# Kernel tuning notes

Hardware: AMD Instinct MI355X
Metric: run time of the kernel (lower is better)

Reference implementation:

```python
import jax, jax.numpy as jnp
import numpy as np
from jax import lax

K = 8          # num_classes
C_IN = 256     # in_channels
EPS = 1e-5


def resize_bilinear_ac(x, H, W):
    """Bilinear resize with align_corners=True. x: [B,C,h,w] -> [B,C,H,W]."""
    B, C, h, w = x.shape
    if h == H and w == W:
        return x
    ys = jnp.linspace(0.0, h - 1.0, H)
    xs = jnp.linspace(0.0, w - 1.0, W)
    y0 = jnp.floor(ys).astype(jnp.int32)
    x0 = jnp.floor(xs).astype(jnp.int32)
    y1 = jnp.minimum(y0 + 1, h - 1)
    x1 = jnp.minimum(x0 + 1, w - 1)
    wy = (ys - y0.astype(x.dtype))[None, None, :, None]
    wx = (xs - x0.astype(x.dtype))[None, None, None, :]
    g00 = x[:, :, y0][:, :, :, x0]
    g01 = x[:, :, y0][:, :, :, x1]
    g10 = x[:, :, y1][:, :, :, x0]
    g11 = x[:, :, y1][:, :, :, x1]
    top = g00 * (1.0 - wx) + g01 * wx
    bot = g10 * (1.0 - wx) + g11 * wx
    return top * (1.0 - wy) + bot * wy


def setup_inputs() -> dict:
    key = jax.random.key(0)
    ks = jax.random.split(key, 16)
    shapes = [(2, 256, 128, 128), (2, 256, 64, 64), (2, 256, 32, 32), (2, 256, 16, 16), (2, 256, 8, 8)]
    inp = {}
    for i, s in enumerate(shapes):
        inp[f"feat{i}"] = jax.random.normal(ks[i], s, dtype=jnp.float32)
    inp["attr_feat"] = jax.random.normal(ks[5], (2, K * C_IN, 64, 64), dtype=jnp.float32)
    # learned params
    inp["mlp_f_w"] = jax.random.normal(ks[6], (256, 256), dtype=jnp.float32) * 0.02
    inp["mlp_f_b"] = jnp.zeros((256,), dtype=jnp.float32)
    inp["mlp_a_w"] = jax.random.normal(ks[7], (256, 256), dtype=jnp.float32) * 0.02
    inp["mlp_a_b"] = jnp.zeros((256,), dtype=jnp.float32)
    # 5 grouped convs: [out=2048, in_per_group=256, 3, 3] each, no bias (BN follows)
    inp["conv_w"] = jax.random.normal(ks[8], (5, K * C_IN, C_IN, 3, 3), dtype=jnp.float32) * 0.02
    inp["bn_gamma"] = jnp.ones((5, K * C_IN), dtype=jnp.float32)
    inp["bn_beta"] = jnp.zeros((5, K * C_IN), dtype=jnp.float32)
    inp["bn_mean"] = jax.random.normal(ks[9], (5, K * C_IN), dtype=jnp.float32) * 0.1
    inp["bn_var"] = jax.random.uniform(ks[10], (5, K * C_IN), dtype=jnp.float32, minval=0.5, maxval=1.5)
    return inp


def _forward(feats, attr_feat, mlp_f_w, mlp_f_b, mlp_a_w, mlp_a_b, conv_w, bn_gamma, bn_beta, bn_mean, bn_var):
    B = attr_feat.shape[0]
    # global avg pool attr -> [B, K, C] -> mlp_a
    avg_attr = attr_feat.mean(axis=(2, 3)).reshape(B, K, C_IN)
    avg_attr = avg_attr @ mlp_a_w.T + mlp_a_b  # [B,K,256]
    outs = []
    for i, x in enumerate(feats):
        _, C, H, W = x.shape
        avg_x = x.mean(axis=(2, 3)) @ mlp_f_w.T + mlp_f_b          # [B,256]
        logits = jnp.einsum('bkc,bc->bk', avg_attr, avg_x)          # [B,K]
        attn = jax.nn.softmax(logits, axis=-1)
        y = resize_bilinear_ac(attr_feat, H, W)                      # [B,2048,H,W]
        y = lax.conv_general_dilated(
            y, conv_w[i], window_strides=(1, 1), padding=((1, 1), (1, 1)),
            dimension_numbers=('NCHW', 'OIHW', 'NCHW'), feature_group_count=K)
        inv = lax.rsqrt(bn_var[i] + EPS)
        y = (y - bn_mean[i][None, :, None, None]) * (inv * bn_gamma[i])[None, :, None, None] + bn_beta[i][None, :, None, None]
        y = jax.nn.relu(y)
        y = y.reshape(B, K, C, H, W)
        y = jnp.einsum('bkchw,bk->bchw', y, attn)                   # weighted sum over classes
        outs.append(jax.nn.relu(x + y))
    return tuple(outs)


def reference(feat0, feat1, feat2, feat3, feat4, attr_feat, mlp_f_w, mlp_f_b, mlp_a_w, mlp_a_b, conv_w, bn_gamma, bn_beta, bn_mean, bn_var):
    feats = [feat0, feat1, feat2, feat3, feat4]
    return _forward(feats, attr_feat, mlp_f_w, mlp_f_b, mlp_a_w, mlp_a_b, conv_w, bn_gamma, bn_beta, bn_mean, bn_var)
```

## Files before the change

kernel.cpp:

```cpp
#include <hip/hip_runtime.h>
#include <hip/hip_bf16.h>
#include <cstdint>

typedef __attribute__((ext_vector_type(8))) short short8;
typedef __attribute__((ext_vector_type(4))) float f32x4;

#define EPSV 1e-5f

__device__ __forceinline__ void gload_lds16(const void* g, void* l) {
  __builtin_amdgcn_global_load_lds(
      (const __attribute__((address_space(1))) void*)(uintptr_t)g,
      (__attribute__((address_space(3))) void*)(uint32_t)(uintptr_t)l,
      16, 0, 0);
}

__device__ __forceinline__ uint32_t f2bf_rne(float v) {
  const uint32_t u = __float_as_uint(v);
  const uint32_t r = ((u >> 16) & 1u) + 0x7fffu;
  return (u + r) >> 16;
}

__global__ void mean_kernel(const float* __restrict__ in, float* __restrict__ out,
                            int HW, float inv) {
  const int ch = blockIdx.x;
  const int t = threadIdx.x;
  const float* p = in + (size_t)ch * HW;
  float s = 0.f;
  const int nv = HW >> 2;
  const float4* pv = (const float4*)p;
  for (int i = t; i < nv; i += 256) { float4 v = pv[i]; s += v.x + v.y + v.z + v.w; }
  __shared__ float red[256];
  red[t] = s; __syncthreads();
  for (int off = 128; off > 0; off >>= 1) {
    if (t < off) red[t] += red[t + off];
    __syncthreads();
  }
  if (t == 0) out[ch] = red[0] * inv;
}

__global__ void wtrans_kernel(const float* __restrict__ cw,
                              const float* __restrict__ gamma, const float* __restrict__ beta,
                              const float* __restrict__ mean, const float* __restrict__ var,
                              __hip_bfloat16* __restrict__ wt, float* __restrict__ bias) {
  const int oc = blockIdx.x;
  const int i  = blockIdx.y;
  const int ci = threadIdx.x;
  const int idx = i * 2048 + oc;
  const float sc = rsqrtf(var[idx] + EPSV) * gamma[idx];
  if (ci == 0) bias[idx] = beta[idx] - mean[idx] * sc;
  const int g = oc >> 8, co = oc & 255;
  const float* src = cw + ((size_t)idx * 256 + ci) * 9;
  const size_t dbase = (size_t)(i * 8 + g) * 9 * 65536 + co * 256 + ci;
#pragma unroll
  for (int tap = 0; tap < 9; ++tap)
    wt[dbase + (size_t)tap * 65536] = __float2bfloat16(src[tap] * sc);
}

__global__ void gate_kernel(const float* __restrict__ meanA, const float* __restrict__ meanF,
                            const float* __restrict__ Wa, const float* __restrict__ ba,
                            const float* __restrict__ Wf, const float* __restrict__ bfp,
                            float* __restrict__ attn) {
  __shared__ float mA[16 * 256];
  __shared__ float mF[10 * 256];
  __shared__ float pA[16 * 256];
  __shared__ float pF[10 * 256];
  __shared__ float lg[80];
  const int t = threadIdx.x;
  for (int i = t; i < 4096; i += 256) mA[i] = meanA[i];
  for (int i = t; i < 2560; i += 256) mF[i] = meanF[i];
  __syncthreads();
  {
    float acc[16];
#pragma unroll
    for (int j = 0; j < 16; ++j) acc[j] = 0.f;
    for (int ci = 0; ci < 256; ++ci) {
      const float w = Wa[t * 256 + ci];
#pragma unroll
      for (int j = 0; j < 16; ++j) acc[j] += mA[j * 256 + ci] * w;
    }
    const float bb = ba[t];
#pragma unroll
    for (int j = 0; j < 16; ++j) pA[j * 256 + t] = acc[j] + bb;
  }
  {
    float acc[10];
#pragma unroll
    for (int j = 0; j < 10; ++j) acc[j] = 0.f;
    for (int ci = 0; ci < 256; ++ci) {
      const float w = Wf[t * 256 + ci];
#pragma unroll
      for (int j = 0; j < 10; ++j) acc[j] += mF[j * 256 + ci] * w;
    }
    const float bb = bfp[t];
#pragma unroll
    for (int j = 0; j < 10; ++j) pF[j * 256 + t] = acc[j] + bb;
  }
  __syncthreads();
  if (t < 80) {
    const int i = t >> 4, r = t & 15, b = r >> 3, k = r & 7;
    const float* a = &pA[(b * 8 + k) * 256];
    const float* f = &pF[(i * 2 + b) * 256];
    float d = 0.f;
    for (int c = 0; c < 256; ++c) d += a[c] * f[c];
    lg[t] = d;
  }
  __syncthreads();
  if (t < 10) {
    const int base = t * 8;
    float m = lg[base];
    for (int k = 1; k < 8; ++k) m = fmaxf(m, lg[base + k]);
    float e[8], s = 0.f;
    for (int k = 0; k < 8; ++k) { e[k] = __expf(lg[base + k] - m); s += e[k]; }
    const float invs = 1.f / s;
    for (int k = 0; k < 8; ++k) attn[base + k] = e[k] * invs;
  }
}

__global__ void resize_kernel(const float* __restrict__ attr,
                              __hip_bfloat16* __restrict__ R,
                              int W, int Hp, int Wp, float scl) {
  const int bk = blockIdx.x;
  const int yp = blockIdx.y;
  const int t  = threadIdx.x;
  const size_t rowbase = ((size_t)bk * Hp + yp) * (size_t)Wp * 256;
  if (yp == 0 || yp == Hp - 1) {
    uint32_t* p = (uint32_t*)(R + rowbase);
    const int n = Wp * 128;
    for (int idx = t; idx < n; idx += 256) p[idx] = 0u;
    return;
  }
  const int y = yp - 1;
  const float fy = y * scl;
  int y0 = (int)floorf(fy); if (y0 > 63) y0 = 63;
  const float wy = fy - (float)y0;
  const int y1 = min(y0 + 1, 63);
  __shared__ float buf[2][64][65];
  const int cc = t >> 2, seg = (t & 3) * 16;
  const int bb = bk >> 3, k = bk & 7;
  const float* ab = attr + (size_t)bb * 2048 * 4096;
  const int ci = t & 63;
  for (int cq = 0; cq < 4; ++cq) {
    __syncthreads();
    {
      const int ch = k * 256 + cq * 64 + cc;
      const float* r0 = ab + ((size_t)ch * 64 + y0) * 64;
      const float* r1 = ab + ((size_t)ch * 64 + y1) * 64;
#pragma unroll
      for (int u = 0; u < 4; ++u) {
        float4 v0 = ((const float4*)r0)[(t & 3) * 4 + u];
        float4 v1 = ((const float4*)r1)[(t & 3) * 4 + u];
        buf[0][cc][seg + u * 4 + 0] = v0.x; buf[0][cc][seg + u * 4 + 1] = v0.y;
        buf[0][cc][seg + u * 4 + 2] = v0.z; buf[0][cc][seg + u * 4 + 3] = v0.w;
        buf[1][cc][seg + u * 4 + 0] = v1.x; buf[1][cc][seg + u * 4 + 1] = v1.y;
        buf[1][cc][seg + u * 4 + 2] = v1.z; buf[1][cc][seg + u * 4 + 3] = v1.w;
      }
    }
    __syncthreads();
    for (int x = t >> 6; x < W; x += 4) {
      const float fx = x * scl;
      int x0 = (int)floorf(fx); if (x0 > 63) x0 = 63;
      const float wx = fx - (float)x0;
      const int x1 = min(x0 + 1, 63);
      const float top = buf[0][ci][x0] * (1.f - wx) + buf[0][ci][x1] * wx;
      const float bot = buf[1][ci][x0] * (1.f - wx) + buf[1][ci][x1] * wx;
      R[rowbase + (size_t)(x + 1) * 256 + cq * 64 + ci] = __float2bfloat16(top * (1.f - wy) + bot * wy);
    }
    if (t < 64) {
      R[rowbase + cq * 64 + t] = __float2bfloat16(0.f);
      R[rowbase + (size_t)(Wp - 1) * 256 + cq * 64 + t] = __float2bfloat16(0.f);
    }
  }
}

__device__ __forceinline__ void coords36(int u, int g0, int& g, int& ty, int& tx, int& cq) {
  g = g0 + u / 36;
  const int r = u % 36;
  const int tap = r >> 2;
  cq = r & 3;
  ty = tap / 3;
  tx = tap - ty * 3;
}

__global__ __launch_bounds__(512, 1)
void conv256_kernel(const __hip_bfloat16* __restrict__ R,
                    const __hip_bfloat16* __restrict__ Wt,
                    const float* __restrict__ bias,
                    const float* __restrict__ attn,
                    __hip_bfloat16* __restrict__ zout,
                    int W, int lw, int Hp, int Wp, int HW,
                    int NB, int b0) {
  __shared__ alignas(16) __hip_bfloat16 ldsA[2][256 * 64];
  __shared__ alignas(16) __hip_bfloat16 ldsB[2][256 * 64];
  __shared__ float biasL[256];
  const int tid  = threadIdx.x;
  const int lane = tid & 63;
  const int wave = __builtin_amdgcn_readfirstlane(tid >> 6);
  const int wm = (wave >> 2) * 128;
  const int wn = (wave & 3) * 64;

  const int X = gridDim.x;
  const int T = X * (int)gridDim.y;
  int lin = (int)blockIdx.x + X * (int)blockIdx.y;
  if ((T & 7) == 0) lin = (lin & 7) * (T >> 3) + (lin >> 3);
  const int yv = lin / X, xp = lin - yv * X;
  const int n0 = xp * 256;
  const int bb = yv % NB;
  const int g0 = yv / NB;

  const int c8 = lane & 7, r8 = lane >> 3;
  const int swz = (c8 ^ r8) << 3;
  const int aoff0 = ((wave * 32 + r8) << 8) + swz;
  const int dst0  = wave * 2048;
  int boff[4];
#pragma unroll
  for (int q = 0; q < 4; ++q) {
    const int row = wave * 32 + q * 8 + r8;
    const int n = n0 + row;
    const int y = n >> lw, x = n & (W - 1);
    boff[q] = ((y * Wp + x) << 8) + swz;
  }

  const size_t rgstride = (size_t)Hp * Wp * 256;
  const __hip_bfloat16* Rg = R + (size_t)(bb * 8 + g0) * rgstride;
  const __hip_bfloat16* Wg = Wt + ((size_t)g0 * 9 << 16);

  if (tid < 256) biasL[tid] = bias[(g0 << 8) + tid];
  const float aw = attn[(b0 + bb) * 8 + g0];
  __syncthreads();

  const f32x4 fz = {0.f, 0.f, 0.f, 0.f};
  f32x4 acc[8][4];
#pragma unroll
  for (int mf = 0; mf < 8; ++mf)
#pragma unroll
    for (int nf = 0; nf < 4; ++nf) acc[mf][nf] = fz;

#define ISSUE_KT(t_)                                                           \
  {                                                                            \
    const int tap_ = (t_) >> 2, cq_ = (t_) & 3;                                \
    const int ty_ = (tap_ >= 6) ? 2 : (tap_ >= 3 ? 1 : 0);                     \
    const int tx_ = tap_ - ty_ * 3;                                            \
    const __hip_bfloat16* wp = Wg + ((size_t)tap_ << 16) + (cq_ << 6);         \
    const __hip_bfloat16* rp = Rg + ((ty_ * Wp + tx_) << 8) + (cq_ << 6);      \
    const int sl_ = (t_) & 1;                                                  \
    _Pragma("unroll")                                                          \
    for (int q = 0; q < 4; ++q) {                                              \
      gload_lds16(wp + aoff0 + q * 2048, &ldsA[sl_][dst0 + q * 512]);          \
      gload_lds16(rp + boff[q], &ldsB[sl_][dst0 + q * 512]);                   \
    }                                                                          \
  }

  ISSUE_KT(0);

  const int l15 = lane & 15, cb0 = lane >> 4;
  for (int t = 0; t < 36; ++t) {
    if (t + 1 < 36) {
      ISSUE_KT(t + 1);
      asm volatile("s_waitcnt vmcnt(8)" ::: "memory");
    } else {
      asm volatile("s_waitcnt vmcnt(0)" ::: "memory");
    }
    __builtin_amdgcn_s_barrier();
    asm volatile("" ::: "memory");

    const __hip_bfloat16* pA = &ldsA[t & 1][0];
    const __hip_bfloat16* pB = &ldsB[t & 1][0];

    short8 bfv[8], afA[4], afB[4];
#pragma unroll
    for (int ks = 0; ks < 2; ++ks)
#pragma unroll
      for (int nf = 0; nf < 4; ++nf) {
        const int row = wn + nf * 16 + l15;
        bfv[ks * 4 + nf] =
            *(const short8*)&pB[(row << 6) + (((ks * 4 + cb0) ^ (row & 7)) << 3)];
      }
#pragma unroll
    for (int m = 0; m < 4; ++m) {
      const int row = wm + m * 16 + l15;
      afA[m] = *(const short8*)&pA[(row << 6) + ((cb0 ^ (row & 7)) << 3)];
    }
#pragma unroll
    for (int m = 0; m < 4; ++m) {
      const int row = wm + 64 + m * 16 + l15;
      afB[m] = *(const short8*)&pA[(row << 6) + ((cb0 ^ (row & 7)) << 3)];
    }
    __builtin_amdgcn_sched_barrier(0);
    __builtin_amdgcn_s_setprio(1);
#pragma unroll
    for (int m = 0; m < 4; ++m)
#pragma unroll
      for (int nf = 0; nf < 4; ++nf)
        acc[m][nf] = __builtin_amdgcn_mfma_f32_16x16x32_bf16(
            afA[m], bfv[nf], acc[m][nf], 0, 0, 0);
    __builtin_amdgcn_s_setprio(0);
#pragma unroll
    for (int m = 0; m < 4; ++m) {
      const int row = wm + m * 16 + l15;
      afA[m] = *(const short8*)&pA[(row << 6) + (((4 + cb0) ^ (row & 7)) << 3)];
    }
    __builtin_amdgcn_sched_barrier(0);
    __builtin_amdgcn_s_setprio(1);
#pragma unroll
    for (int m = 0; m < 4; ++m)
#pragma unroll
      for (int nf = 0; nf < 4; ++nf)
        acc[4 + m][nf] = __builtin_amdgcn_mfma_f32_16x16x32_bf16(
            afB[m], bfv[nf], acc[4 + m][nf], 0, 0, 0);
    __builtin_amdgcn_s_setprio(0);
#pragma unroll
    for (int m = 0; m < 4; ++m) {
      const int row = wm + 64 + m * 16 + l15;
      afB[m] = *(const short8*)&pA[(row << 6) + (((4 + cb0) ^ (row & 7)) << 3)];
    }
    __builtin_amdgcn_sched_barrier(0);
    __builtin_amdgcn_s_setprio(1);
#pragma unroll
    for (int m = 0; m < 4; ++m)
#pragma unroll
      for (int nf = 0; nf < 4; ++nf)
        acc[m][nf] = __builtin_amdgcn_mfma_f32_16x16x32_bf16(
            afA[m], bfv[4 + nf], acc[m][nf], 0, 0, 0);
#pragma unroll
    for (int m = 0; m < 4; ++m)
#pragma unroll
      for (int nf = 0; nf < 4; ++nf)
        acc[4 + m][nf] = __builtin_amdgcn_mfma_f32_16x16x32_bf16(
            afB[m], bfv[4 + nf], acc[4 + m][nf], 0, 0, 0);
    __builtin_amdgcn_s_setprio(0);
    __builtin_amdgcn_s_barrier();
    asm volatile("" ::: "memory");
  }
#undef ISSUE_KT

  __hip_bfloat16* zb = zout + (size_t)yv * 256 * (size_t)HW;
#pragma unroll
  for (int mf = 0; mf < 8; ++mf) {
    const int cobase = wm + mf * 16 + (cb0 << 2);
#pragma unroll
    for (int r = 0; r < 4; ++r) {
      const float bs = biasL[cobase + r];
      __hip_bfloat16* zr = zb + (size_t)(cobase + r) * HW;
#pragma unroll
      for (int nf = 0; nf < 4; ++nf) {
        const int n = n0 + wn + nf * 16 + l15;
        zr[n] = __float2bfloat16(aw * fmaxf(acc[mf][nf][r] + bs, 0.f));
      }
    }
  }
}

__global__ __launch_bounds__(256, 2)
void conv_kernel(const __hip_bfloat16* __restrict__ R,
                 const __hip_bfloat16* __restrict__ Wt,
                 const float* __restrict__ bias,
                 const float* __restrict__ attn,
                 const float* __restrict__ featp,
                 void* __restrict__ outp,
                 int W, int lw, int Hp, int Wp, int HW,
                 int b0, int NB, int gcount) {
  __shared__ alignas(16) __hip_bfloat16 ldsA[2][128 * 64];
  __shared__ alignas(16) __hip_bfloat16 ldsB[3][128 * 64];
  const int tid  = threadIdx.x;
  const int lane = tid & 63;
  const int wave = __builtin_amdgcn_readfirstlane(tid >> 6);
  const int wm = (wave >> 1) * 64;
  const int wn = (wave & 1) * 64;

  const int nx  = gridDim.x;
  const int lin = blockIdx.x;
  const int pos = ((nx & 7) == 0) ? ((lin & 7) * (nx >> 3) + (lin >> 3)) : lin;
  const int co0 = (pos & 1) * 128;
  const int n0  = (pos >> 1) * 128;

  const int bb  = (int)blockIdx.y % NB;
  const int gs  = (int)blockIdx.y / NB;
  const int b   = b0 + bb;
  const int g0  = gs * gcount;

  const int c8 = lane & 7;
  const int r8 = lane >> 3;
  int aoff[4], boff[4], dst[4];
#pragma unroll
  for (int q = 0; q < 4; ++q) {
    const int row = (wave * 4 + q) * 8 + r8;
    const int sc = (c8 ^ (row & 7)) << 3;
    aoff[q] = ((co0 + row) << 8) + sc;
    int sg = n0 + row; if (sg >= HW) sg = HW - 1;
    const int y = sg >> lw, x = sg & (W - 1);
    boff[q] = ((y * Wp + x) << 8) + sc;
    dst[q] = (wave * 4 + q) * 512;
  }

  const size_t rgstride = (size_t)Hp * Wp * 256;
  const __hip_bfloat16* Rb = R + (size_t)bb * 8 * rgstride;

  const f32x4 fz = {0.f, 0.f, 0.f, 0.f};
  f32x4 fin[4][4], acc[4][4];
#pragma unroll
  for (int mf = 0; mf < 4; ++mf)
#pragma unroll
    for (int nf = 0; nf < 4; ++nf) { fin[mf][nf] = fz; acc[mf][nf] = fz; }

  const int nstages = gcount * 36;
  {
    int g, ty, tx, cq;
    coords36(0, g0, g, ty, tx, cq);
    const __hip_bfloat16* wp = Wt + (((size_t)g * 9 + ty * 3 + tx) << 16) + (cq << 6);
    const __hip_bfloat16* rp = Rb + (size_t)g * rgstride + ((ty * Wp + tx) << 8) + (cq << 6);
#pragma unroll
    for (int q = 0; q < 4; ++q) gload_lds16(wp + aoff[q], &ldsA[0][dst[q]]);
#pragma unroll
    for (int q = 0; q < 4; ++q) gload_lds16(rp + boff[q], &ldsB[0][dst[q]]);
    coords36(1 < nstages ? 1 : 0, g0, g, ty, tx, cq);
    const __hip_bfloat16* rp1 = Rb + (size_t)g * rgstride + ((ty * Wp + tx) << 8) + (cq << 6);
#pragma unroll
    for (int q = 0; q < 4; ++q) gload_lds16(rp1 + boff[q], &ldsB[1][dst[q]]);
  }

  int bcur = 0, b2 = 2;
  int foldc = 0, gcur = g0;

  for (int s = 0; s < nstages; ++s) {
    __builtin_amdgcn_s_barrier();
    asm volatile("" ::: "memory");
    if (s + 1 < nstages) {
      int g, ty, tx, cq;
      coords36(s + 1, g0, g, ty, tx, cq);
      const __hip_bfloat16* wp = Wt + (((size_t)g * 9 + ty * 3 + tx) << 16) + (cq << 6);
      __hip_bfloat16* dA = &ldsA[(s + 1) & 1][0];
#pragma unroll
      for (int q = 0; q < 4; ++q) gload_lds16(wp + aoff[q], dA + dst[q]);
    }
    if (s + 2 < nstages) {
      int g, ty, tx, cq;
      coords36(s + 2, g0, g, ty, tx, cq);
      const __hip_bfloat16* rp = Rb + (size_t)g * rgstride + ((ty * Wp + tx) << 8) + (cq << 6);
      __hip_bfloat16* dB = &ldsB[b2][0];
#pragma unroll
      for (int q = 0; q < 4; ++q) gload_lds16(rp + boff[q], dB + dst[q]);
    }
    if (s + 2 < nstages)      asm volatile("s_waitcnt vmcnt(12)" ::: "memory");
    else if (s + 1 < nstages) asm volatile("s_waitcnt vmcnt(8)" ::: "memory");
    else                      asm volatile("s_waitcnt vmcnt(0)" ::: "memory");
    __builtin_amdgcn_s_barrier();
    asm volatile("" ::: "memory");

    const __hip_bfloat16* pA = &ldsA[s & 1][0];
    const __hip_bfloat16* pB = &ldsB[bcur][0];
#pragma unroll
    for (int ks = 0; ks < 2; ++ks) {
      short8 af[4], bfv[4];
      const int cb = ks * 4 + (lane >> 4);
#pragma unroll
      for (int mf = 0; mf < 4; ++mf) {
        const int row = wm + mf * 16 + (lane & 15);
        af[mf] = *(const short8*)&pA[(row << 6) + ((cb ^ (row & 7)) << 3)];
      }
#pragma unroll
      for (int nf = 0; nf < 4; ++nf) {
        const int row = wn + nf * 16 + (lane & 15);
        bfv[nf] = *(const short8*)&pB[(row << 6) + ((cb ^ (row & 7)) << 3)];
      }
#pragma unroll
      for (int mf = 0; mf < 4; ++mf)
#pragma unroll
        for (int nf = 0; nf < 4; ++nf)
          acc[mf][nf] = __builtin_amdgcn_mfma_f32_16x16x32_bf16(
              af[mf], bfv[nf], acc[mf][nf], 0, 0, 0);
    }

    if (++bcur == 3) bcur = 0;
    if (++b2 == 3) b2 = 0;

    if (++foldc == 36) {
      foldc = 0;
      const float aw = attn[b * 8 + gcur];
#pragma unroll
      for (int mf = 0; mf < 4; ++mf) {
        const int cobase = co0 + wm + mf * 16 + ((lane >> 4) << 2);
#pragma unroll
        for (int r = 0; r < 4; ++r) {
          const float bs = bias[(gcur << 8) + cobase + r];
#pragma unroll
          for (int nf = 0; nf < 4; ++nf) {
            fin[mf][nf][r] += aw * fmaxf(acc[mf][nf][r] + bs, 0.f);
            acc[mf][nf][r] = 0.f;
          }
        }
      }
      ++gcur;
    }
  }

  const size_t plane = (size_t)256 * HW;
  if (featp) {
    const float* fb = featp + (size_t)b * plane;
    float* ob = (float*)outp + (size_t)b * plane;
#pragma unroll
    for (int mf = 0; mf < 4; ++mf) {
      const int cobase = co0 + wm + mf * 16 + ((lane >> 4) << 2);
#pragma unroll
      for (int nf = 0; nf < 4; ++nf) {
        const int n = n0 + wn + nf * 16 + (lane & 15);
        if (n < HW) {
#pragma unroll
          for (int r = 0; r < 4; ++r) {
            const size_t idx = (size_t)(cobase + r) * HW + n;
            ob[idx] = fmaxf(fb[idx] + fin[mf][nf][r], 0.f);
          }
        }
      }
    }
  } else {
    __hip_bfloat16* zb = (__hip_bfloat16*)outp + ((size_t)gs * 2 + b) * plane;
#pragma unroll
    for (int mf = 0; mf < 4; ++mf) {
      const int cobase = co0 + wm + mf * 16 + ((lane >> 4) << 2);
#pragma unroll
      for (int nf = 0; nf < 4; ++nf) {
        const int n = n0 + wn + nf * 16 + (lane & 15);
        if (n < HW) {
#pragma unroll
          for (int r = 0; r < 4; ++r)
            zb[(size_t)(cobase + r) * HW + n] = __float2bfloat16(fin[mf][nf][r]);
        }
      }
    }
  }
}

__global__ void reduce_kernel(const __hip_bfloat16* __restrict__ z,
                              const float* __restrict__ feat,
                              float* __restrict__ outp, int total, int S) {
  const int i4 = (blockIdx.x * 256 + threadIdx.x) * 4;
  if (i4 >= total) return;
  float4 f = *(const float4*)(feat + i4);
  float s0 = f.x, s1 = f.y, s2 = f.z, s3 = f.w;
  for (int j = 0; j < S; ++j) {
    const ushort4 v = *(const ushort4*)(z + (size_t)j * total + i4);
    s0 += __uint_as_float((uint32_t)v.x << 16);
    s1 += __uint_as_float((uint32_t)v.y << 16);
    s2 += __uint_as_float((uint32_t)v.z << 16);
    s3 += __uint_as_float((uint32_t)v.w << 16);
  }
  float4 o = {fmaxf(s0, 0.f), fmaxf(s1, 0.f), fmaxf(s2, 0.f), fmaxf(s3, 0.f)};
  *(float4*)(outp + i4) = o;
}

extern "C" void kernel_launch(void* const* d_in, const int* in_sizes, int n_in,
                              void* d_out, int out_size, void* d_ws, size_t ws_size,
                              hipStream_t stream) {
  const float* feat[5];
  for (int i = 0; i < 5; ++i) feat[i] = (const float*)d_in[i];
  const float* attr = (const float*)d_in[5];
  const float* mfw = (const float*)d_in[6];
  const float* mfb = (const float*)d_in[7];
  const float* maw = (const float*)d_in[8];
  const float* mab = (const float*)d_in[9];
  const float* cw  = (const float*)d_in[10];
  const float* bng = (const float*)d_in[11];
  const float* bnb = (const float*)d_in[12];
  const float* bnm = (const float*)d_in[13];
  const float* bnv = (const float*)d_in[14];
  float* out = (float*)d_out;

  char* ws = (char*)d_ws;
  float* attnW = (float*)(ws);
  float* meanA = (float*)(ws + 512);
  float* meanF = (float*)(ws + 20480);
  float* biasW = (float*)(ws + 32768);
  __hip_bfloat16* Wt = (__hip_bfloat16*)(ws + 131072);
  const size_t R_OFF = 47316992;
  __hip_bfloat16* Rbuf = (__hip_bfloat16*)(ws + R_OFF);
  __hip_bfloat16* zbuf = (__hip_bfloat16*)(ws + R_OFF + (size_t)69222400);

  const bool full = ws_size >= (size_t)219316224;

  static const int HS[5] = {128, 64, 32, 16, 8};
  static const size_t OOFF[5] = {0, 8388608, 10485760, 11010048, 11141120};

  mean_kernel<<<4096, 256, 0, stream>>>(attr, meanA, 4096, 1.f / 4096.f);
  for (int i = 0; i < 5; ++i) {
    const int HW = HS[i] * HS[i];
    mean_kernel<<<512, 256, 0, stream>>>(feat[i], meanF + i * 512, HW, 1.f / (float)HW);
  }
  wtrans_kernel<<<dim3(2048, 5), 256, 0, stream>>>(cw, bng, bnb, bnm, bnv, Wt, biasW);
  gate_kernel<<<1, 256, 0, stream>>>(meanA, meanF, maw, mab, mfw, mfb, attnW);

  for (int i = 0; i < 5; ++i) {
    const int H = HS[i], W = H, HW = H * W, Hp = H + 2, Wp = W + 2;
    const int lw = 31 - __builtin_clz((unsigned)W);
    const float scl = 63.f / (float)(H - 1);

    if (full) {
      if (i == 0) {
        const size_t plane = (size_t)256 * HW;
        for (int b0 = 0; b0 < 2; ++b0) {
          resize_kernel<<<dim3(8, Hp), 256, 0, stream>>>(
              attr + (size_t)b0 * 2048 * 4096, Rbuf, W, Hp, Wp, scl);
          conv256_kernel<<<dim3(HW / 256, 8), 512, 0, stream>>>(
              Rbuf, Wt, biasW, attnW, zbuf, W, lw, Hp, Wp, HW, 1, b0);
          reduce_kernel<<<((int)plane / 4 + 255) / 256, 256, 0, stream>>>(
              zbuf, feat[0] + b0 * plane, out + OOFF[0] + b0 * plane, (int)plane, 8);
        }
      } else if (i == 1) {
        resize_kernel<<<dim3(16, Hp), 256, 0, stream>>>(attr, Rbuf, W, Hp, Wp, scl);
        conv256_kernel<<<dim3(HW / 256, 16), 512, 0, stream>>>(
            Rbuf, Wt + (size_t)1 * 8 * 9 * 65536, biasW + 2048, attnW + 16,
            zbuf, W, lw, Hp, Wp, HW, 2, 0);
        const int total = 2 * 256 * HW;
        reduce_kernel<<<(total / 4 + 255) / 256, 256, 0, stream>>>(
            zbuf, feat[1], out + OOFF[1], total, 8);
      } else {
        resize_kernel<<<dim3(16, Hp), 256, 0, stream>>>(attr, Rbuf, W, Hp, Wp, scl);
        const int ntiles = (HW + 127) / 128;
        conv_kernel<<<dim3(ntiles * 2, 16), 256, 0, stream>>>(
            Rbuf, Wt + (size_t)i * 8 * 9 * 65536, biasW + i * 2048, attnW + i * 16,
            nullptr, zbuf, W, lw, Hp, Wp, HW, 0, 2, 1);
        const int total = 2 * 256 * HW;
        reduce_kernel<<<(total / 4 + 255) / 256, 256, 0, stream>>>(
            zbuf, feat[i], out + OOFF[i], total, 8);
      }
    } else {
      const int ntiles = (HW + 127) / 128;
      for (int b0 = 0; b0 < 2; ++b0) {
        resize_kernel<<<dim3(8, Hp), 256, 0, stream>>>(
            attr + (size_t)b0 * 2048 * 4096, Rbuf, W, Hp, Wp, scl);
        conv_kernel<<<dim3(ntiles * 2, 1), 256, 0, stream>>>(
            Rbuf, Wt + (size_t)i * 8 * 9 * 65536, biasW + i * 2048, attnW + i * 16,
            feat[i], out + OOFF[i], W, lw, Hp, Wp, HW, b0, 1, 8);
      }
    }
  }
}
```

Before: 745.5 us.

## Pretranspose attr to NHWC bf16 once and resize from it; stage weight transform via LDS

Adds a one-time kernel that converts attr_feat from NCHW fp32 to an NHWC bf16 copy. Every per-level resize then reads contiguous channel vectors from this half-size buffer instead of doing strided fp32 gathers over the original. The weight-transform kernel now stages each output channel's 2304 weights through LDS, so global reads are coalesced. The cost is an extra pass over attr plus more workspace, and interpolating from bf16-rounded inputs adds a little rounding error.

```diff
diff --git a/kernel.cpp b/kernel.cpp
--- a/kernel.cpp
+++ b/kernel.cpp
@@ -18,6 +18,9 @@
   const uint32_t u = __float_as_uint(v);
   const uint32_t r = ((u >> 16) & 1u) + 0x7fffu;
   return (u + r) >> 16;
+}
+__device__ __forceinline__ float bf2f(uint32_t u) {
+  return __uint_as_float(u << 16);
 }
 
 __global__ void mean_kernel(const float* __restrict__ in, float* __restrict__ out,
@@ -42,18 +45,21 @@
                               const float* __restrict__ gamma, const float* __restrict__ beta,
                               const float* __restrict__ mean, const float* __restrict__ var,
                               __hip_bfloat16* __restrict__ wt, float* __restrict__ bias) {
+  __shared__ float wl[2304];
   const int oc = blockIdx.x;
   const int i  = blockIdx.y;
-  const int ci = threadIdx.x;
+  const int t  = threadIdx.x;
   const int idx = i * 2048 + oc;
+  const float* src = cw + (size_t)idx * 2304;
+  for (int e = t; e < 2304; e += 256) wl[e] = src[e];
+  __syncthreads();
   const float sc = rsqrtf(var[idx] + EPSV) * gamma[idx];
-  if (ci == 0) bias[idx] = beta[idx] - mean[idx] * sc;
+  if (t == 0) bias[idx] = beta[idx] - mean[idx] * sc;
   const int g = oc >> 8, co = oc & 255;
-  const float* src = cw + ((size_t)idx * 256 + ci) * 9;
-  const size_t dbase = (size_t)(i * 8 + g) * 9 * 65536 + co * 256 + ci;
+  const size_t dbase = (size_t)(i * 8 + g) * 9 * 65536 + co * 256 + t;
 #pragma unroll
   for (int tap = 0; tap < 9; ++tap)
-    wt[dbase + (size_t)tap * 65536] = __float2bfloat16(src[tap] * sc);
+    wt[dbase + (size_t)tap * 65536] = __float2bfloat16(wl[t * 9 + tap] * sc);
 }
 
 __global__ void gate_kernel(const float* __restrict__ meanA, const float* __restrict__ meanF,
@@ -113,6 +119,83 @@
     for (int k = 0; k < 8; ++k) { e[k] = __expf(lg[base + k] - m); s += e[k]; }
     const float invs = 1.f / s;
     for (int k = 0; k < 8; ++k) attn[base + k] = e[k] * invs;
+  }
+}
+
+__global__ void tonhwc_kernel(const float* __restrict__ attr,
+                              __hip_bfloat16* __restrict__ A64) {
+  __shared__ float lds[64 * 261];
+  const int bk = blockIdx.x, y = blockIdx.y, t = threadIdx.x;
+  const int b = bk >> 3, k = bk & 7;
+  const float* src = attr + (size_t)(b * 2048 + k * 256) * 4096 + y * 64;
+  for (int e = t; e < 16384; e += 256) {
+    const int ch = e >> 6, x = e & 63;
+    lds[x * 261 + ch] = src[(size_t)ch * 4096 + x];
+  }
+  __syncthreads();
+  __hip_bfloat16* dst = A64 + ((size_t)bk * 64 + y) * 64 * 256;
+  const int ci4 = (t & 63) * 4;
+  for (int x = t >> 6; x < 64; x += 4) {
+    short4 st;
+    st.x = (short)f2bf_rne(lds[x * 261 + ci4 + 0]);
+    st.y = (short)f2bf_rne(lds[x * 261 + ci4 + 1]);
+    st.z = (short)f2bf_rne(lds[x * 261 + ci4 + 2]);
+    st.w = (short)f2bf_rne(lds[x * 261 + ci4 + 3]);
+    *(short4*)&dst[x * 256 + ci4] = st;
+  }
+}
+
+__global__ void resize_nhwc_kernel(const __hip_bfloat16* __restrict__ A64,
+                                   __hip_bfloat16* __restrict__ R,
+                                   int W, int Hp, int Wp, float scl, int bk0) {
+  const int bkl = blockIdx.x;
+  const int yp = blockIdx.y;
+  const int t  = threadIdx.x;
+  const size_t rowbase = ((size_t)bkl * Hp + yp) * (size_t)Wp * 256;
+  if (yp == 0 || yp == Hp - 1) {
+    uint32_t* p = (uint32_t*)(R + rowbase);
+    const int n = Wp * 128;
+    for (int idx = t; idx < n; idx += 256) p[idx] = 0u;
+    return;
+  }
+  const int y = yp - 1;
+  const float fy = y * scl;
+  int y0 = (int)floorf(fy); if (y0 > 63) y0 = 63;
+  const float wy = fy - (float)y0;
+  const int y1 = min(y0 + 1, 63);
+  const __hip_bfloat16* r0 = A64 + ((size_t)(bk0 + bkl) * 64 + y0) * 64 * 256;
+  const __hip_bfloat16* r1 = A64 + ((size_t)(bk0 + bkl) * 64 + y1) * 64 * 256;
+  const int ci4 = (t & 63) * 4;
+  for (int x = t >> 6; x < W; x += 4) {
+    const float fx = x * scl;
+    int x0 = (int)floorf(fx); if (x0 > 63) x0 = 63;
+    const float wx = fx - (float)x0;
+    const int x1 = min(x0 + 1, 63);
+    const ushort4 a00 = *(const ushort4*)&r0[x0 * 256 + ci4];
+    const ushort4 a01 = *(const ushort4*)&r0[x1 * 256 + ci4];
+    const ushort4 a10 = *(const ushort4*)&r1[x0 * 256 + ci4];
+    const ushort4 a11 = *(const ushort4*)&r1[x1 * 256 + ci4];
+    short4 st;
+    {
+      const float top0 = bf2f(a00.x) * (1.f - wx) + bf2f(a01.x) * wx;
+      const float bot0 = bf2f(a10.x) * (1.f - wx) + bf2f(a11.x) * wx;
+      st.x = (short)f2bf_rne(top0 * (1.f - wy) + bot0 * wy);
+      const float top1 = bf2f(a00.y) * (1.f - wx) + bf2f(a01.y) * wx;
+      const float bot1 = bf2f(a10.y) * (1.f - wx) + bf2f(a11.y) * wx;
+      st.y = (short)f2bf_rne(top1 * (1.f - wy) + bot1 * wy);
+      const float top2 = bf2f(a00.z) * (1.f - wx) + bf2f(a01.z) * wx;
+      const float bot2 = bf2f(a10.z) * (1.f - wx) + bf2f(a11.z) * wx;
+      st.z = (short)f2bf_rne(top2 * (1.f - wy) + bot2 * wy);
+      const float top3 = bf2f(a00.w) * (1.f - wx) + bf2f(a01.w) * wx;
+      const float bot3 = bf2f(a10.w) * (1.f - wx) + bf2f(a11.w) * wx;
+      st.w = (short)f2bf_rne(top3 * (1.f - wy) + bot3 * wy);
+    }
+    *(short4*)&R[rowbase + (size_t)(x + 1) * 256 + ci4] = st;
+  }
+  if (t < 64) {
+    const short4 z4 = {0, 0, 0, 0};
+    *(short4*)&R[rowbase + t * 4] = z4;
+    *(short4*)&R[rowbase + (size_t)(Wp - 1) * 256 + t * 4] = z4;
   }
 }
 
@@ -539,10 +622,10 @@
   float s0 = f.x, s1 = f.y, s2 = f.z, s3 = f.w;
   for (int j = 0; j < S; ++j) {
     const ushort4 v = *(const ushort4*)(z + (size_t)j * total + i4);
-    s0 += __uint_as_float((uint32_t)v.x << 16);
-    s1 += __uint_as_float((uint32_t)v.y << 16);
-    s2 += __uint_as_float((uint32_t)v.z << 16);
-    s3 += __uint_as_float((uint32_t)v.w << 16);
+    s0 += bf2f(v.x);
+    s1 += bf2f(v.y);
+    s2 += bf2f(v.z);
+    s3 += bf2f(v.w);
   }
   float4 o = {fmaxf(s0, 0.f), fmaxf(s1, 0.f), fmaxf(s2, 0.f), fmaxf(s3, 0.f)};
   *(float4*)(outp + i4) = o;
@@ -574,6 +657,7 @@
   const size_t R_OFF = 47316992;
   __hip_bfloat16* Rbuf = (__hip_bfloat16*)(ws + R_OFF);
   __hip_bfloat16* zbuf = (__hip_bfloat16*)(ws + R_OFF + (size_t)69222400);
+  __hip_bfloat16* A64  = (__hip_bfloat16*)(ws + R_OFF + (size_t)69222400 + 67108864);
 
   const bool full = ws_size >= (size_t)219316224;
 
@@ -587,6 +671,7 @@
   }
   wtrans_kernel<<<dim3(2048, 5), 256, 0, stream>>>(cw, bng, bnb, bnm, bnv, Wt, biasW);
   gate_kernel<<<1, 256, 0, stream>>>(meanA, meanF, maw, mab, mfw, mfb, attnW);
+  if (full) tonhwc_kernel<<<dim3(16, 64), 256, 0, stream>>>(attr, A64);
 
   for (int i = 0; i < 5; ++i) {
     const int H = HS[i], W = H, HW = H * W, Hp = H + 2, Wp = W + 2;
@@ -597,15 +682,16 @@
       if (i == 0) {
         const size_t plane = (size_t)256 * HW;
         for (int b0 = 0; b0 < 2; ++b0) {
-          resize_kernel<<<dim3(8, Hp), 256, 0, stream>>>(
-              attr + (size_t)b0 * 2048 * 4096, Rbuf, W, Hp, Wp, scl);
+          resize_nhwc_kernel<<<dim3(8, Hp), 256, 0, stream>>>(
+              A64, Rbuf, W, Hp, Wp, scl, b0 * 8);
           conv256_kernel<<<dim3(HW / 256, 8), 512, 0, stream>>>(
               Rbuf, Wt, biasW, attnW, zbuf, W, lw, Hp, Wp, HW, 1, b0);
           reduce_kernel<<<((int)plane / 4 + 255) / 256, 256, 0, stream>>>(
               zbuf, feat[0] + b0 * plane, out + OOFF[0] + b0 * plane, (int)plane, 8);
         }
       } else if (i == 1) {
-        resize_kernel<<<dim3(16, Hp), 256, 0, stream>>>(attr, Rbuf, W, Hp, Wp, scl);
+        resize_nhwc_kernel<<<dim3(16, Hp), 256, 0, stream>>>(
+            A64, Rbuf, W, Hp, Wp, scl, 0);
         conv256_kernel<<<dim3(HW / 256, 16), 512, 0, stream>>>(
             Rbuf, Wt + (size_t)1 * 8 * 9 * 65536, biasW + 2048, attnW + 16,
             zbuf, W, lw, Hp, Wp, HW, 2, 0);
@@ -613,7 +699,8 @@
         reduce_kernel<<<(total / 4 + 255) / 256, 256, 0, stream>>>(
             zbuf, feat[1], out + OOFF[1], total, 8);
       } else {
-        resize_kernel<<<dim3(16, Hp), 256, 0, stream>>>(attr, Rbuf, W, Hp, Wp, scl);
+        resize_nhwc_kernel<<<dim3(16, Hp), 256, 0, stream>>>(
+            A64, Rbuf, W, Hp, Wp, scl, 0);
         const int ntiles = (HW + 127) / 128;
         conv_kernel<<<dim3(ntiles * 2, 16), 256, 0, stream>>>(
             Rbuf, Wt + (size_t)i * 8 * 9 * 65536, biasW + i * 2048, attnW + i * 16,
```

Result: slower. 772.9 us (+3.7%).
